# Kernel optimization log

Measured on AMD Instinct MI355X. Metric: run time of the kernel, lower is better.

The kernel has to match this reference:

```python
import jax, jax.numpy as jnp
import numpy as np

C = 128; D_INNER = 256; D_STATE = 16; D_CONV = 4; DT_RANK = 8; SCALE_MLP = 2


def layernorm(x, g, b, eps=1e-5):
    m = x.mean(-1, keepdims=True)
    v = ((x - m) ** 2).mean(-1, keepdims=True)
    return (x - m) * jax.lax.rsqrt(v + eps) * g + b


def causal_conv(x, w, b):
    # x: (B, L, D); w: (D, K) depthwise causal conv; b: (D,)
    K = w.shape[1]
    xt = x.transpose(0, 2, 1)  # (B, D, L)
    out = jax.lax.conv_general_dilated(
        xt, w[:, None, :], (1,), [(K - 1, 0)],
        dimension_numbers=("NCH", "OIH", "NCH"), feature_group_count=w.shape[0])
    return (out + b[None, :, None]).transpose(0, 2, 1)


def selective_scan(u, delta, A, Bm, Cm, Dv):
    # u, delta: (B, L, D); A: (D, N); Bm, Cm: (B, L, N); Dv: (D,)
    def step(h, inp):
        u_t, d_t, B_t, C_t = inp  # (B,D),(B,D),(B,N),(B,N)
        dA = jnp.exp(d_t[..., None] * A)                      # (B, D, N)
        h = dA * h + (d_t * u_t)[..., None] * B_t[:, None, :]  # (B, D, N)
        y = jnp.einsum("bdn,bn->bd", h, C_t)
        return h, y
    Bsz, L, Din = u.shape
    h0 = jnp.zeros((Bsz, Din, A.shape[1]), u.dtype)
    inputs = (u.transpose(1, 0, 2), delta.transpose(1, 0, 2),
              Bm.transpose(1, 0, 2), Cm.transpose(1, 0, 2))
    _, ys = jax.lax.scan(step, h0, inputs)
    return ys.transpose(1, 0, 2) + u * Dv


def mamba_branch(xc, z, cw, cb, Wx_, Wdt_, bdt_, Al, Dv):
    u = jax.nn.silu(causal_conv(xc, cw, cb))
    xdbl = u @ Wx_.T  # (B, L, dt_rank + 2*d_state)
    dr = Wdt_.shape[1]; ds = Al.shape[1]
    dt = jax.nn.softplus(xdbl[..., :dr] @ Wdt_.T + bdt_)
    Bm = xdbl[..., dr:dr + ds]
    Cm = xdbl[..., dr + ds:]
    y = selective_scan(u, dt, -jnp.exp(Al), Bm, Cm, Dv)
    return y * jax.nn.silu(z)


def setup_inputs():
    key = jax.random.key(0)
    ks = jax.random.split(key, 20)
    w = lambda k, shape, s=0.02: jax.random.normal(k, shape, jnp.float32) * s
    A_log = jnp.log(jnp.tile(jnp.arange(1, D_STATE + 1, dtype=jnp.float32), (D_INNER, 1)))
    dt_bias = jnp.full((D_INNER,), jnp.log(jnp.expm1(0.01)), jnp.float32)
    return dict(
        x=jax.random.normal(ks[0], (4, 256, 64, C), jnp.float32),
        g1=jnp.ones((C,), jnp.float32), b1=jnp.zeros((C,), jnp.float32),
        W_in=w(ks[1], (2 * D_INNER, C)),
        conv_w=w(ks[2], (D_INNER, D_CONV), 0.2), conv_b=jnp.zeros((D_INNER,), jnp.float32),
        Wx=w(ks[3], (DT_RANK + 2 * D_STATE, D_INNER)),
        Wdt=w(ks[4], (D_INNER, DT_RANK), 0.1), bdt=dt_bias,
        A_log=A_log, D=jnp.ones((D_INNER,), jnp.float32),
        conv_wb=w(ks[5], (D_INNER, D_CONV), 0.2), conv_bb=jnp.zeros((D_INNER,), jnp.float32),
        Wxb=w(ks[6], (DT_RANK + 2 * D_STATE, D_INNER)),
        Wdtb=w(ks[7], (D_INNER, DT_RANK), 0.1), bdtb=dt_bias,
        A_b_log=A_log, D_b=jnp.ones((D_INNER,), jnp.float32),
        W_out=w(ks[8], (C, D_INNER)),
        g2=jnp.ones((C,), jnp.float32), b2=jnp.zeros((C,), jnp.float32),
        g3=jnp.ones((C,), jnp.float32), b3=jnp.zeros((C,), jnp.float32),
        W1m=w(ks[9], (C, SCALE_MLP * C)), b1m=jnp.zeros((SCALE_MLP * C,), jnp.float32),
        W2m=w(ks[10], (SCALE_MLP * C, C)), b2m=jnp.zeros((C,), jnp.float32),
    )


def reference(x, g1, b1, W_in, conv_w, conv_b, Wx, Wdt, bdt, A_log, D,
              conv_wb, conv_bb, Wxb, Wdtb, bdtb, A_b_log, D_b, W_out,
              g2, b2, g3, b3, W1m, b1m, W2m, b2m):
    B, T, N, Cc = x.shape
    xs = x.transpose(0, 2, 1, 3).reshape(B * N, T, Cc)
    # --- CustomBiMamba: LN -> (Dropout eval=identity) -> BiMamba v2 -> LN, residual ---
    h = layernorm(xs, g1, b1)
    xz = h @ W_in.T  # (B*N, T, 2*d_inner)
    xc, z = jnp.split(xz, 2, axis=-1)
    y_f = mamba_branch(xc, z, conv_w, conv_b, Wx, Wdt, bdt, A_log, D)
    y_b = mamba_branch(xc[:, ::-1], z[:, ::-1], conv_wb, conv_bb, Wxb, Wdtb, bdtb,
                       A_b_log, D_b)[:, ::-1]
    y = (y_f + y_b) @ W_out.T
    y = layernorm(y, g2, b2)
    xs = y + xs
    xo = xs.reshape(B, N, T, Cc).transpose(0, 2, 1, 3)
    # --- MLP residual ---
    h2 = layernorm(xo, g3, b3)
    mlp = jax.nn.gelu(h2 @ W1m + b1m, approximate=False) @ W2m + b2m
    return xo + mlp
```

## Files before the change

kernel.cpp:

```cpp
#include <hip/hip_runtime.h>
#include <hip/hip_bf16.h>
#include <math.h>

#define CC 128
#define DI 256
#define SSEQ 256
#define ROWS 65536

typedef __hip_bfloat16 bf16;
typedef __attribute__((ext_vector_type(8))) short short8;
typedef __attribute__((ext_vector_type(4))) float float4v;
typedef __attribute__((ext_vector_type(2))) float f32x2;

__device__ __forceinline__ float to_f(float v) { return v; }
__device__ __forceinline__ float to_f(bf16 v)  { return __bfloat162float(v); }
__device__ __forceinline__ bf16  f2b(float v)  { return __float2bfloat16(v); }
__device__ __forceinline__ float bf2f_bits(short v) {
    union { unsigned u; float f; } c; c.u = ((unsigned)(unsigned short)v) << 16; return c.f;
}
__device__ __forceinline__ f32x2 mk2(float a, float b) { f32x2 r; r.x = a; r.y = b; return r; }
__device__ __forceinline__ f32x2 fma2(f32x2 a, f32x2 b, f32x2 c) { return a * b + c; }

__device__ __forceinline__ float wave_sum(float v) {
    #pragma unroll
    for (int o = 1; o < 64; o <<= 1) v += __shfl_xor(v, o, 64);
    return v;
}
__device__ __forceinline__ float silu_f(float x) {
    return x * __builtin_amdgcn_rcpf(1.f + __expf(-x));
}
__device__ __forceinline__ float gelu_f(float x) { return 0.5f * x * (1.f + erff(x * 0.70710678118654752f)); }
__device__ __forceinline__ float softplus_f(float x) {
    return (x > 20.f) ? x : __logf(1.f + __expf(x));
}

__global__ __launch_bounds__(256) void ln1_kernel(const float* __restrict__ x,
                                                  const float* __restrict__ g,
                                                  const float* __restrict__ b,
                                                  bf16* __restrict__ out) {
    int wave = threadIdx.x >> 6, lane = threadIdx.x & 63;
    int r = blockIdx.x * 4 + wave;
    int s = r >> 8, t = r & 255;
    int bb = s >> 6, n = s & 63;
    size_t xbase = (((size_t)(bb * 256 + t)) * 64 + n) * CC;
    float v0 = x[xbase + lane], v1 = x[xbase + lane + 64];
    float s1 = wave_sum(v0 + v1);
    float s2 = wave_sum(v0 * v0 + v1 * v1);
    float m = s1 * (1.f / 128.f);
    float var = s2 * (1.f / 128.f) - m * m;
    float rstd = rsqrtf(var + 1e-5f);
    size_t ob = (size_t)r * CC;
    out[ob + lane]      = f2b((v0 - m) * rstd * g[lane]      + b[lane]);
    out[ob + lane + 64] = f2b((v1 - m) * rstd * g[lane + 64] + b[lane + 64]);
// ... 210 lines not shown
        {
            int n = tid >> 2, part = tid & 3;
            if (n < 48) {
                bf16 tmp[8];
                #pragma unroll
                for (int j = 0; j < 8; j++)
                    tmp[j] = (n < 40) ? f2b(Wx[(size_t)n * 256 + k0 + part * 8 + j]) : f2b(0.f);
                *(uint4*)&Bs[n][part * 8] = *(uint4*)tmp;
            }
        }
        __syncthreads();
        short8 a = *(const short8*)&As[wv * 16 + lrow][lk];
        #pragma unroll
        for (int jt = 0; jt < 3; jt++) {
            short8 bfr = *(const short8*)&Bs[jt * 16 + lrow][lk];
            acc[jt] = __builtin_amdgcn_mfma_f32_16x16x32_bf16(a, bfr, acc[jt], 0, 0, 0);
        }
        __syncthreads();
    }
    #pragma unroll
    for (int jt = 0; jt < 3; jt++) {
        int col = jt * 16 + lrow;
        if (col < 40) {
            #pragma unroll
            for (int r = 0; r < 4; r++) {
                int row = t0 + wv * 16 + quad * 4 + r;
                C[(size_t)(s * 256 + row) * 40 + col] = f2b(acc[jt][r]);
            }
        }
    }
}


#define LOADROW(R, T) do {                                                  \
    const float4* rp_ = (const float4*)(rows + (T) * 40);                   \
    R##0 = rp_[0]; R##1 = rp_[1]; R##2 = rp_[2]; R##3 = rp_[3];             \
    R##4 = rp_[4]; R##5 = rp_[5]; R##6 = rp_[6]; R##7 = rp_[7];             \
    R##8 = rp_[8]; R##9 = rp_[9];                                           \
} while (0)

#define SCAN_STEP(T, R) do {                                                \
    float u_ = uc0; uc0 = uc1;                                              \
    if ((T) + 2 < 256) { uc1 = to_f(*unext); unext += ystep; }              \
    f32x2 acc2 = mk2((R##0).x, (R##0).y) * wdt01;                           \
    acc2 = fma2(mk2((R##0).z, (R##0).w), wdt23, acc2);                      \
    acc2 = fma2(mk2((R##1).x, (R##1).y), wdt45, acc2);                      \
    acc2 = fma2(mk2((R##1).z, (R##1).w), wdt67, acc2);                      \
    float dtr_ = bd + acc2.x + acc2.y;                                      \
    float dt_ = softplus_f(dtr_);                                           \
    float du_ = dt_ * u_;                                                   \
    float d1 = __expf(dt_ * A0);                                            \
    float d2v = d1 * d1;                                                    \
    f32x2 pw0 = mk2(d1, d2v);                                               \
    f32x2 dd2 = mk2(d2v, d2v);                                              \
    f32x2 pw1 = pw0 * dd2, pw2 = pw1 * dd2, pw3 = pw2 * dd2;                \
    f32x2 dd8 = mk2(pw3.y, pw3.y);                                          \
    f32x2 pw4 = pw0 * dd8, pw5 = pw1 * dd8, pw6 = pw2 * dd8, pw7 = pw3 * dd8; \
    f32x2 du2 = mk2(du_, du_);                                              \
    hp0 = fma2(pw0, hp0, du2 * mk2((R##2).x, (R##2).y));                    \
    hp1 = fma2(pw1, hp1, du2 * mk2((R##2).z, (R##2).w));                    \
    hp2 = fma2(pw2, hp2, du2 * mk2((R##3).x, (R##3).y));                    \
    hp3 = fma2(pw3, hp3, du2 * mk2((R##3).z, (R##3).w));                    \
    hp4 = fma2(pw4, hp4, du2 * mk2((R##4).x, (R##4).y));                    \
    hp5 = fma2(pw5, hp5, du2 * mk2((R##4).z, (R##4).w));                    \
    hp6 = fma2(pw6, hp6, du2 * mk2((R##5).x, (R##5).y));                    \
    hp7 = fma2(pw7, hp7, du2 * mk2((R##5).z, (R##5).w));                    \
    f32x2 ya = hp0 * mk2((R##6).x, (R##6).y);                               \
    f32x2 yb = hp1 * mk2((R##6).z, (R##6).w);                               \
    ya = fma2(hp2, mk2((R##7).x, (R##7).y), ya);                            \
    yb = fma2(hp3, mk2((R##7).z, (R##7).w), yb);                            \
    ya = fma2(hp4, mk2((R##8).x, (R##8).y), ya);                            \
    yb = fma2(hp5, mk2((R##8).z, (R##8).w), yb);                            \
    ya = fma2(hp6, mk2((R##9).x, (R##9).y), ya);                            \
    yb = fma2(hp7, mk2((R##9).z, (R##9).w), yb);                            \
    f32x2 ys = ya + yb;                                                     \
    float yv_ = ys.x + ys.y + u_ * Dd;                                      \
    *yp = f2b(yv_); yp += ystep;                                            \
} while (0)

__global__ __launch_bounds__(256) void scan_kernel(
        const bf16* __restrict__ xdbl_f, const bf16* __restrict__ xdbl_b,
        const float* __restrict__ Wdt_f, const float* __restrict__ bdt_f,
        const float* __restrict__ Alog_f, const float* __restrict__ D_f,
        const float* __restrict__ Wdt_b, const float* __restrict__ bdt_b,
        const float* __restrict__ Alog_b, const float* __restrict__ D_b,
        bf16* __restrict__ YF, bf16* __restrict__ YB) {
    __shared__ float rows[256 * 40];
    int tid = threadIdx.x;
    int dir = blockIdx.x >> 8;
    int s = blockIdx.x & 255;
    int d = tid;

    const bf16* xd = (dir ? xdbl_b : xdbl_f) + (size_t)s * 10240;
    #pragma unroll
    for (int i = 0; i < 5; i++) {
        int idx = i * 256 + tid;
        uint4 v = ((const uint4*)xd)[idx];
        short8 sv = *(short8*)&v;
        float f[8];
        #pragma unroll
        for (int j = 0; j < 8; j++) f[j] = bf2f_bits(sv[j]);
        *(float4*)&rows[idx * 8]     = *(float4*)&f[0];
        *(float4*)&rows[idx * 8 + 4] = *(float4*)&f[4];
    }

    const float* Alog = dir ? Alog_b : Alog_f;
    const float* Wdtp = dir ? Wdt_b  : Wdt_f;
    float Aarr[16];
    #pragma unroll
    for (int n = 0; n < 16; n++) Aarr[n] = -__expf(Alog[d * 16 + n]);
    f32x2 wdt01 = mk2(Wdtp[d * 8 + 0], Wdtp[d * 8 + 1]);
    f32x2 wdt23 = mk2(Wdtp[d * 8 + 2], Wdtp[d * 8 + 3]);
    f32x2 wdt45 = mk2(Wdtp[d * 8 + 4], Wdtp[d * 8 + 5]);
    f32x2 wdt67 = mk2(Wdtp[d * 8 + 6], Wdtp[d * 8 + 7]);
    float bd = dir ? bdt_b[d] : bdt_f[d];
    float Dd = dir ? D_b[d]   : D_f[d];
    bf16* Y = dir ? YB : YF;

    float A0 = Aarr[0];
    int pw = 1;
    #pragma unroll
    for (int n = 1; n < 16; n++)
        pw &= (fabsf(Aarr[n] - (float)(n + 1) * A0) <= 1e-4f * fabsf(Aarr[n]) + 1e-6f) ? 1 : 0;
    pw = __all(pw);
    __syncthreads();

    bf16* yp = Y + ((size_t)(s * 256 + (dir ? 255 : 0))) * 256 + d;
    ptrdiff_t ystep = dir ? -256 : 256;
    float uc0 = to_f(*yp);
    float uc1 = to_f(*(yp + ystep));
    const bf16* unext = yp + 2 * ystep;

    if (pw) {
        f32x2 hp0 = {}, hp1 = {}, hp2 = {}, hp3 = {},
              hp4 = {}, hp5 = {}, hp6 = {}, hp7 = {};
        float4 ra0, ra1, ra2, ra3, ra4, ra5, ra6, ra7, ra8, ra9;
        float4 rb0, rb1, rb2, rb3, rb4, rb5, rb6, rb7, rb8, rb9;
        LOADROW(ra, 0);
        #pragma unroll 1
        for (int t = 0; t < 256; t += 2) {
            LOADROW(rb, t + 1);
            SCAN_STEP(t, ra);
            if (t + 2 < 256) LOADROW(ra, t + 2);
            SCAN_STEP(t + 1, rb);
        }
    } else {
        float h[16];
        #pragma unroll
        for (int n = 0; n < 16; n++) h[n] = 0.f;
        for (int t = 0; t < 256; t++) {
            float u = uc0; uc0 = uc1;
            if (t + 2 < 256) { uc1 = to_f(*unext); unext += ystep; }
            const float* row = rows + t * 40;
            float4 q0 = *(const float4*)(row);
            float4 q1 = *(const float4*)(row + 4);
            float4 qb0 = *(const float4*)(row + 8);
            float4 qb1 = *(const float4*)(row + 12);
            float4 qb2 = *(const float4*)(row + 16);
            float4 qb3 = *(const float4*)(row + 20);
            float4 qc0 = *(const float4*)(row + 24);
            float4 qc1 = *(const float4*)(row + 28);
            float4 qc2 = *(const float4*)(row + 32);
            float4 qc3 = *(const float4*)(row + 36);
            float dtr = bd;
            dtr += q0.x * wdt01.x + q0.y * wdt01.y + q0.z * wdt23.x + q0.w * wdt23.y;
            dtr += q1.x * wdt45.x + q1.y * wdt45.y + q1.z * wdt67.x + q1.w * wdt67.y;
            float dt = softplus_f(dtr);
            float du = dt * u, y = 0.f;
            float Bm[16] = {qb0.x,qb0.y,qb0.z,qb0.w, qb1.x,qb1.y,qb1.z,qb1.w,
                            qb2.x,qb2.y,qb2.z,qb2.w, qb3.x,qb3.y,qb3.z,qb3.w};
            float Cm[16] = {qc0.x,qc0.y,qc0.z,qc0.w, qc1.x,qc1.y,qc1.z,qc1.w,
                            qc2.x,qc2.y,qc2.z,qc2.w, qc3.x,qc3.y,qc3.z,qc3.w};
            #pragma unroll
            for (int n = 0; n < 16; n++) {
                float dA = __expf(dt * Aarr[n]);
                h[n] = dA * h[n] + du * Bm[n];
                y += h[n] * Cm[n];
            }
            y += u * Dd;
            *yp = f2b(y); yp += ystep;
        }
    }
}

extern "C" void kernel_launch(void* const* d_in, const int* in_sizes, int n_in,
                              void* d_out, int out_size, void* d_ws, size_t ws_size,
                              hipStream_t stream) {
    const float* x      = (const float*)d_in[0];
    const float* g1     = (const float*)d_in[1];
    const float* b1     = (const float*)d_in[2];
    const float* W_in   = (const float*)d_in[3];
    const float* conv_w = (const float*)d_in[4];
    const float* conv_b = (const float*)d_in[5];
    const float* Wx     = (const float*)d_in[6];
    const float* Wdt    = (const float*)d_in[7];
    const float* bdt    = (const float*)d_in[8];
    const float* A_log  = (const float*)d_in[9];
    const float* Dvec   = (const float*)d_in[10];
    const float* conv_wb= (const float*)d_in[11];
    const float* conv_bb= (const float*)d_in[12];
    const float* Wxb    = (const float*)d_in[13];
    const float* Wdtb   = (const float*)d_in[14];
    const float* bdtb   = (const float*)d_in[15];
    const float* A_b_log= (const float*)d_in[16];
    const float* D_b    = (const float*)d_in[17];
    const float* W_out  = (const float*)d_in[18];
    const float* g2     = (const float*)d_in[19];
    const float* b2     = (const float*)d_in[20];
    const float* g3     = (const float*)d_in[21];
    const float* b3     = (const float*)d_in[22];
    const float* W1m    = (const float*)d_in[23];
    const float* b1m    = (const float*)d_in[24];
    const float* W2m    = (const float*)d_in[25];
    const float* b2m    = (const float*)d_in[26];

    bf16* ws  = (bf16*)d_ws;
    bf16* XZ  = ws;
    bf16* YF  = ws + 33554432UL;
    bf16* YB  = ws + 50331648UL;
    bf16* H2  = ws;
    bf16* HID = ws + 8388608UL;
    float* out = (float*)d_out;
    bf16* LN1OUT = (bf16*)d_out;
    bf16* XDBL_F = (bf16*)d_out;
    bf16* XDBL_B = (bf16*)d_out + 2621440UL;

    ln1_kernel<<<ROWS / 4, 256, 0, stream>>>(x, g1, b1, LN1OUT);
    mfma_gemm_kernel<true, 0, 4><<<dim3(ROWS / 64, 8), 256, 0, stream>>>(
        LN1OUT, CC, W_in, nullptr, XZ, 512, 512, CC);
    mfma_conv_kernel<0><<<SSEQ * 4, 256, 0, stream>>>(XZ, conv_w, conv_b, Wx, XDBL_F, YF);
    mfma_conv_kernel<1><<<SSEQ * 4, 256, 0, stream>>>(XZ, conv_wb, conv_bb, Wxb, XDBL_B, YB);
    scan_kernel<<<512, 256, 0, stream>>>(XDBL_F, XDBL_B,
        Wdt, bdt, A_log, Dvec, Wdtb, bdtb, A_b_log, D_b, YF, YB);
    mfma_ln2res_kernel<<<ROWS / 64, 256, 0, stream>>>(YF, YB, XZ, W_out, g2, b2, x, out);
    ln3_kernel<<<ROWS / 4, 256, 0, stream>>>(out, g3, b3, H2);
    mfma_gemm_kernel<false, 1, 4><<<dim3(ROWS / 64, 4), 256, 0, stream>>>(
        H2, CC, W1m, b1m, HID, 2 * CC, 2 * CC, CC);
    mfma_gemm_kernel<false, 2, 8><<<dim3(ROWS / 64, 2), 256, 0, stream>>>(
        HID, 2 * CC, W2m, b2m, out, CC, CC, 2 * CC);
}
```

Measured before the change: 522.7 us.

## Split selective scan into two sequence chunks with a carry-correction pass

The selective scan is split into two 128-step halves per sequence and direction, doubling the block count. The second half starts from a zero state and stores a running prefix sum of dt into a reused scratch region of XZ. The first half stores its final hidden state. A new correction kernel then adds C·exp(A·S)·h_end to the second-half outputs. This trades an extra launch, extra global traffic and a bf16 prefix sum for twice the parallelism on the serial scan, which may cost some accuracy.

```diff
diff --git a/kernel.cpp b/kernel.cpp
--- a/kernel.cpp
+++ b/kernel.cpp
@@ -295,22 +295,23 @@
 }
 
 
-#define LOADROW(R, T) do {                                                  \
-    const float4* rp_ = (const float4*)(rows + (T) * 40);                   \
+#define LOADROW(R, J) do {                                                  \
+    const float4* rp_ = (const float4*)(rows + (J) * 40);                   \
     R##0 = rp_[0]; R##1 = rp_[1]; R##2 = rp_[2]; R##3 = rp_[3];             \
     R##4 = rp_[4]; R##5 = rp_[5]; R##6 = rp_[6]; R##7 = rp_[7];             \
     R##8 = rp_[8]; R##9 = rp_[9];                                           \
 } while (0)
 
-#define SCAN_STEP(T, R) do {                                                \
+#define SCAN_STEP(J, R) do {                                                \
     float u_ = uc0; uc0 = uc1;                                              \
-    if ((T) + 2 < 256) { uc1 = to_f(*unext); unext += ystep; }              \
+    if ((J) + 2 < 128) { uc1 = to_f(*unext); unext += ystep; }              \
     f32x2 acc2 = mk2((R##0).x, (R##0).y) * wdt01;                           \
     acc2 = fma2(mk2((R##0).z, (R##0).w), wdt23, acc2);                      \
     acc2 = fma2(mk2((R##1).x, (R##1).y), wdt45, acc2);                      \
     acc2 = fma2(mk2((R##1).z, (R##1).w), wdt67, acc2);                      \
     float dtr_ = bd + acc2.x + acc2.y;                                      \
     float dt_ = softplus_f(dtr_);                                           \
+    if (kk) { Ssum += dt_; *sp = f2b(Ssum); sp += 512; }                    \
     float du_ = dt_ * u_;                                                   \
     float d1 = __expf(dt_ * A0);                                            \
     float d2v = d1 * d1;                                                    \
@@ -341,30 +342,34 @@
     *yp = f2b(yv_); yp += ystep;                                            \
 } while (0)
 
-__global__ __launch_bounds__(256) void scan_kernel(
+__global__ __launch_bounds__(256, 4) void scan1_kernel(
         const bf16* __restrict__ xdbl_f, const bf16* __restrict__ xdbl_b,
         const float* __restrict__ Wdt_f, const float* __restrict__ bdt_f,
         const float* __restrict__ Alog_f, const float* __restrict__ D_f,
         const float* __restrict__ Wdt_b, const float* __restrict__ bdt_b,
         const float* __restrict__ Alog_b, const float* __restrict__ D_b,
-        bf16* __restrict__ YF, bf16* __restrict__ YB) {
-    __shared__ float rows[256 * 40];
+        bf16* __restrict__ YF, bf16* __restrict__ YB,
+        float* __restrict__ Hend, bf16* __restrict__ Sbuf) {
+    __shared__ float rows[128 * 40];
     int tid = threadIdx.x;
-    int dir = blockIdx.x >> 8;
-    int s = blockIdx.x & 255;
+    int s   = blockIdx.x >> 2;
+    int dir = (blockIdx.x >> 1) & 1;
+    int kk  = blockIdx.x & 1;
     int d = tid;
 
-    const bf16* xd = (dir ? xdbl_b : xdbl_f) + (size_t)s * 10240;
-    #pragma unroll
-    for (int i = 0; i < 5; i++) {
+    const bf16* xd = (dir ? xdbl_b : xdbl_f) + ((size_t)(s * 256 + kk * 128)) * 40;
+    #pragma unroll
+    for (int i = 0; i < 3; i++) {
         int idx = i * 256 + tid;
-        uint4 v = ((const uint4*)xd)[idx];
-        short8 sv = *(short8*)&v;
-        float f[8];
-        #pragma unroll
-        for (int j = 0; j < 8; j++) f[j] = bf2f_bits(sv[j]);
-        *(float4*)&rows[idx * 8]     = *(float4*)&f[0];
-        *(float4*)&rows[idx * 8 + 4] = *(float4*)&f[4];
+        if (idx < 640) {
+            uint4 v = ((const uint4*)xd)[idx];
+            short8 sv = *(short8*)&v;
+            float f[8];
+            #pragma unroll
+            for (int j = 0; j < 8; j++) f[j] = bf2f_bits(sv[j]);
+            *(float4*)&rows[idx * 8]     = *(float4*)&f[0];
+            *(float4*)&rows[idx * 8 + 4] = *(float4*)&f[4];
+        }
     }
 
     const float* Alog = dir ? Alog_b : Alog_f;
@@ -388,11 +393,15 @@
     pw = __all(pw);
     __syncthreads();
 
-    bf16* yp = Y + ((size_t)(s * 256 + (dir ? 255 : 0))) * 256 + d;
+    int row0 = dir ? (255 - kk * 128) : (kk * 128);
+    bf16* yp = Y + ((size_t)(s * 256 + row0)) * 256 + d;
     ptrdiff_t ystep = dir ? -256 : 256;
     float uc0 = to_f(*yp);
     float uc1 = to_f(*(yp + ystep));
     const bf16* unext = yp + 2 * ystep;
+
+    float Ssum = 0.f;
+    bf16* sp = Sbuf + ((size_t)(s * 256 + (dir ? 0 : 128))) * 512 + d;
 
     if (pw) {
         f32x2 hp0 = {}, hp1 = {}, hp2 = {}, hp3 = {},
@@ -401,19 +410,30 @@
         float4 rb0, rb1, rb2, rb3, rb4, rb5, rb6, rb7, rb8, rb9;
         LOADROW(ra, 0);
         #pragma unroll 1
-        for (int t = 0; t < 256; t += 2) {
+        for (int t = 0; t < 128; t += 2) {
             LOADROW(rb, t + 1);
             SCAN_STEP(t, ra);
-            if (t + 2 < 256) LOADROW(ra, t + 2);
+            if (t + 2 < 128) LOADROW(ra, t + 2);
             SCAN_STEP(t + 1, rb);
+        }
+        if (kk == 0) {
+            float* hb = Hend + ((size_t)((dir * 256 + s) * 16)) * 256 + d;
+            hb[0 * 256] = hp0.x; hb[1 * 256] = hp0.y;
+            hb[2 * 256] = hp1.x; hb[3 * 256] = hp1.y;
+            hb[4 * 256] = hp2.x; hb[5 * 256] = hp2.y;
+            hb[6 * 256] = hp3.x; hb[7 * 256] = hp3.y;
+            hb[8 * 256] = hp4.x; hb[9 * 256] = hp4.y;
+            hb[10 * 256] = hp5.x; hb[11 * 256] = hp5.y;
+            hb[12 * 256] = hp6.x; hb[13 * 256] = hp6.y;
+            hb[14 * 256] = hp7.x; hb[15 * 256] = hp7.y;
         }
     } else {
         float h[16];
         #pragma unroll
         for (int n = 0; n < 16; n++) h[n] = 0.f;
-        for (int t = 0; t < 256; t++) {
+        for (int t = 0; t < 128; t++) {
             float u = uc0; uc0 = uc1;
-            if (t + 2 < 256) { uc1 = to_f(*unext); unext += ystep; }
+            if (t + 2 < 128) { uc1 = to_f(*unext); unext += ystep; }
             const float* row = rows + t * 40;
             float4 q0 = *(const float4*)(row);
             float4 q1 = *(const float4*)(row + 4);
@@ -429,6 +449,7 @@
             dtr += q0.x * wdt01.x + q0.y * wdt01.y + q0.z * wdt23.x + q0.w * wdt23.y;
             dtr += q1.x * wdt45.x + q1.y * wdt45.y + q1.z * wdt67.x + q1.w * wdt67.y;
             float dt = softplus_f(dtr);
+            if (kk) { Ssum += dt; *sp = f2b(Ssum); sp += 512; }
             float du = dt * u, y = 0.f;
             float Bm[16] = {qb0.x,qb0.y,qb0.z,qb0.w, qb1.x,qb1.y,qb1.z,qb1.w,
                             qb2.x,qb2.y,qb2.z,qb2.w, qb3.x,qb3.y,qb3.z,qb3.w};
@@ -442,6 +463,100 @@
             }
             y += u * Dd;
             *yp = f2b(y); yp += ystep;
+        }
+        if (kk == 0) {
+            float* hb = Hend + ((size_t)((dir * 256 + s) * 16)) * 256 + d;
+            #pragma unroll
+            for (int n = 0; n < 16; n++) hb[n * 256] = h[n];
+        }
+    }
+}
+
+__global__ __launch_bounds__(256, 4) void scan2_kernel(
+        const bf16* __restrict__ xdbl_f, const bf16* __restrict__ xdbl_b,
+        const float* __restrict__ Alog_f, const float* __restrict__ Alog_b,
+        const float* __restrict__ Hend, const bf16* __restrict__ Sbuf,
+        bf16* __restrict__ YF, bf16* __restrict__ YB) {
+    __shared__ float cms[64 * 16];
+    int tid = threadIdx.x;
+    int s   = blockIdx.x >> 2;
+    int dir = (blockIdx.x >> 1) & 1;
+    int jh  = blockIdx.x & 1;
+    int d = tid;
+
+    const bf16* xd = dir ? xdbl_b : xdbl_f;
+    #pragma unroll
+    for (int i = 0; i < 4; i++) {
+        int e = i * 256 + tid;
+        int j = e >> 4, n = e & 15;
+        cms[j * 16 + n] = to_f(xd[((size_t)(s * 256 + 128 + jh * 64 + j)) * 40 + 24 + n]);
+    }
+
+    const float* Alog = dir ? Alog_b : Alog_f;
+    float Aarr[16];
+    #pragma unroll
+    for (int n = 0; n < 16; n++) Aarr[n] = -__expf(Alog[d * 16 + n]);
+    float A0 = Aarr[0];
+    int pw = 1;
+    #pragma unroll
+    for (int n = 1; n < 16; n++)
+        pw &= (fabsf(Aarr[n] - (float)(n + 1) * A0) <= 1e-4f * fabsf(Aarr[n]) + 1e-6f) ? 1 : 0;
+    pw = __all(pw);
+
+    const float* hb = Hend + ((size_t)((dir * 256 + s) * 16)) * 256 + d;
+    f32x2 H0 = mk2(hb[0 * 256], hb[1 * 256]);
+    f32x2 H1 = mk2(hb[2 * 256], hb[3 * 256]);
+    f32x2 H2 = mk2(hb[4 * 256], hb[5 * 256]);
+    f32x2 H3 = mk2(hb[6 * 256], hb[7 * 256]);
+    f32x2 H4 = mk2(hb[8 * 256], hb[9 * 256]);
+    f32x2 H5 = mk2(hb[10 * 256], hb[11 * 256]);
+    f32x2 H6 = mk2(hb[12 * 256], hb[13 * 256]);
+    f32x2 H7 = mk2(hb[14 * 256], hb[15 * 256]);
+    __syncthreads();
+
+    const bf16* sp = Sbuf + ((size_t)(s * 256 + (dir ? 0 : 128) + jh * 64)) * 512 + d;
+    bf16* Y = dir ? YB : YF;
+    bf16* yp = Y + ((size_t)(s * 256 + (dir ? (127 - jh * 64) : (128 + jh * 64)))) * 256 + d;
+    ptrdiff_t ystep = dir ? -256 : 256;
+
+    if (pw) {
+        #pragma unroll 2
+        for (int j = 0; j < 64; j++) {
+            float S = to_f(sp[(size_t)j * 512]);
+            float e1 = __expf(A0 * S);
+            float e2 = e1 * e1;
+            f32x2 pw0 = mk2(e1, e2);
+            f32x2 dd2 = mk2(e2, e2);
+            f32x2 pw1 = pw0 * dd2, pw2 = pw1 * dd2, pw3 = pw2 * dd2;
+            f32x2 dd8 = mk2(pw3.y, pw3.y);
+            f32x2 pw4 = pw0 * dd8, pw5 = pw1 * dd8, pw6 = pw2 * dd8, pw7 = pw3 * dd8;
+            const float4* cmr = (const float4*)(cms + j * 16);
+            float4 c0 = cmr[0], c1 = cmr[1], c2 = cmr[2], c3 = cmr[3];
+            f32x2 acc = (pw0 * H0) * mk2(c0.x, c0.y);
+            acc = fma2(pw1 * H1, mk2(c0.z, c0.w), acc);
+            acc = fma2(pw2 * H2, mk2(c1.x, c1.y), acc);
+            acc = fma2(pw3 * H3, mk2(c1.z, c1.w), acc);
+            acc = fma2(pw4 * H4, mk2(c2.x, c2.y), acc);
+            acc = fma2(pw5 * H5, mk2(c2.z, c2.w), acc);
+            acc = fma2(pw6 * H6, mk2(c3.x, c3.y), acc);
+            acc = fma2(pw7 * H7, mk2(c3.z, c3.w), acc);
+            float corr = acc.x + acc.y;
+            bf16* ya = yp + (ptrdiff_t)j * ystep;
+            *ya = f2b(to_f(*ya) + corr);
+        }
+    } else {
+        float h0v[16];
+        #pragma unroll
+        for (int n = 0; n < 16; n++) h0v[n] = hb[n * 256];
+        #pragma unroll 2
+        for (int j = 0; j < 64; j++) {
+            float S = to_f(sp[(size_t)j * 512]);
+            float corr = 0.f;
+            #pragma unroll
+            for (int n = 0; n < 16; n++)
+                corr += cms[j * 16 + n] * __expf(Aarr[n] * S) * h0v[n];
+            bf16* ya = yp + (ptrdiff_t)j * ystep;
+            *ya = f2b(to_f(*ya) + corr);
         }
     }
 }
@@ -487,14 +602,17 @@
     bf16* LN1OUT = (bf16*)d_out;
     bf16* XDBL_F = (bf16*)d_out;
     bf16* XDBL_B = (bf16*)d_out + 2621440UL;
+    float* HEND  = (float*)((char*)d_out + (16UL << 20));
 
     ln1_kernel<<<ROWS / 4, 256, 0, stream>>>(x, g1, b1, LN1OUT);
     mfma_gemm_kernel<true, 0, 4><<<dim3(ROWS / 64, 8), 256, 0, stream>>>(
         LN1OUT, CC, W_in, nullptr, XZ, 512, 512, CC);
     mfma_conv_kernel<0><<<SSEQ * 4, 256, 0, stream>>>(XZ, conv_w, conv_b, Wx, XDBL_F, YF);
     mfma_conv_kernel<1><<<SSEQ * 4, 256, 0, stream>>>(XZ, conv_wb, conv_bb, Wxb, XDBL_B, YB);
-    scan_kernel<<<512, 256, 0, stream>>>(XDBL_F, XDBL_B,
-        Wdt, bdt, A_log, Dvec, Wdtb, bdtb, A_b_log, D_b, YF, YB);
+    scan1_kernel<<<1024, 256, 0, stream>>>(XDBL_F, XDBL_B,
+        Wdt, bdt, A_log, Dvec, Wdtb, bdtb, A_b_log, D_b, YF, YB, HEND, XZ);
+    scan2_kernel<<<1024, 256, 0, stream>>>(XDBL_F, XDBL_B, A_log, A_b_log,
+        HEND, XZ, YF, YB);
     mfma_ln2res_kernel<<<ROWS / 64, 256, 0, stream>>>(YF, YB, XZ, W_out, g2, b2, x, out);
     ln3_kernel<<<ROWS / 4, 256, 0, stream>>>(out, g3, b3, H2);
     mfma_gemm_kernel<false, 1, 4><<<dim3(ROWS / 64, 4), 256, 0, stream>>>(
```

After: 698.5 us. 33.6% more time.

## Split selective scan over two sequence halves with carry-state correction pass

Applied to the files above, without the earlier changes.

The scan kernel now uses 512 threads per block, with each half of the threads scanning 128 timesteps of the sequence from a zero state. The first half writes its final hidden state to shared memory. The second half then runs a correction pass that decays this carried state through its own steps and adds the C-weighted contribution to its outputs. The aim is to double the parallelism of the sequential scan on a launch that has only 512 blocks. The cost is recomputing dt and the decays and rereading and rewriting the second-half outputs, and the correction pass runs serially after the barrier.

```diff
diff --git a/kernel.cpp b/kernel.cpp
--- a/kernel.cpp
+++ b/kernel.cpp
@@ -302,9 +302,9 @@
     R##8 = rp_[8]; R##9 = rp_[9];                                           \
 } while (0)
 
-#define SCAN_STEP(T, R) do {                                                \
+#define SCAN_STEP(J, R) do {                                                \
     float u_ = uc0; uc0 = uc1;                                              \
-    if ((T) + 2 < 256) { uc1 = to_f(*unext); unext += ystep; }              \
+    if ((J) + 2 < 128) { uc1 = to_f(*unext); unext += ystep; }              \
     f32x2 acc2 = mk2((R##0).x, (R##0).y) * wdt01;                           \
     acc2 = fma2(mk2((R##0).z, (R##0).w), wdt23, acc2);                      \
     acc2 = fma2(mk2((R##1).x, (R##1).y), wdt45, acc2);                      \
@@ -329,19 +329,19 @@
     hp6 = fma2(pw6, hp6, du2 * mk2((R##5).x, (R##5).y));                    \
     hp7 = fma2(pw7, hp7, du2 * mk2((R##5).z, (R##5).w));                    \
     f32x2 ya = hp0 * mk2((R##6).x, (R##6).y);                               \
-    f32x2 yb = hp1 * mk2((R##6).z, (R##6).w);                               \
+    f32x2 yb2 = hp1 * mk2((R##6).z, (R##6).w);                              \
     ya = fma2(hp2, mk2((R##7).x, (R##7).y), ya);                            \
-    yb = fma2(hp3, mk2((R##7).z, (R##7).w), yb);                            \
+    yb2 = fma2(hp3, mk2((R##7).z, (R##7).w), yb2);                          \
     ya = fma2(hp4, mk2((R##8).x, (R##8).y), ya);                            \
-    yb = fma2(hp5, mk2((R##8).z, (R##8).w), yb);                            \
+    yb2 = fma2(hp5, mk2((R##8).z, (R##8).w), yb2);                          \
     ya = fma2(hp6, mk2((R##9).x, (R##9).y), ya);                            \
-    yb = fma2(hp7, mk2((R##9).z, (R##9).w), yb);                            \
-    f32x2 ys = ya + yb;                                                     \
+    yb2 = fma2(hp7, mk2((R##9).z, (R##9).w), yb2);                          \
+    f32x2 ys = ya + yb2;                                                    \
     float yv_ = ys.x + ys.y + u_ * Dd;                                      \
     *yp = f2b(yv_); yp += ystep;                                            \
 } while (0)
 
-__global__ __launch_bounds__(256) void scan_kernel(
+__global__ __launch_bounds__(512, 4) void scan_kernel(
         const bf16* __restrict__ xdbl_f, const bf16* __restrict__ xdbl_b,
         const float* __restrict__ Wdt_f, const float* __restrict__ bdt_f,
         const float* __restrict__ Alog_f, const float* __restrict__ D_f,
@@ -349,22 +349,26 @@
         const float* __restrict__ Alog_b, const float* __restrict__ D_b,
         bf16* __restrict__ YF, bf16* __restrict__ YB) {
     __shared__ float rows[256 * 40];
+    __shared__ float hbuf[16 * 256];
     int tid = threadIdx.x;
     int dir = blockIdx.x >> 8;
     int s = blockIdx.x & 255;
-    int d = tid;
+    int half = tid >> 8;
+    int d = tid & 255;
 
     const bf16* xd = (dir ? xdbl_b : xdbl_f) + (size_t)s * 10240;
     #pragma unroll
-    for (int i = 0; i < 5; i++) {
-        int idx = i * 256 + tid;
-        uint4 v = ((const uint4*)xd)[idx];
-        short8 sv = *(short8*)&v;
-        float f[8];
-        #pragma unroll
-        for (int j = 0; j < 8; j++) f[j] = bf2f_bits(sv[j]);
-        *(float4*)&rows[idx * 8]     = *(float4*)&f[0];
-        *(float4*)&rows[idx * 8 + 4] = *(float4*)&f[4];
+    for (int i = 0; i < 3; i++) {
+        int idx = i * 512 + tid;
+        if (idx < 1280) {
+            uint4 v = ((const uint4*)xd)[idx];
+            short8 sv = *(short8*)&v;
+            float f[8];
+            #pragma unroll
+            for (int j = 0; j < 8; j++) f[j] = bf2f_bits(sv[j]);
+            *(float4*)&rows[idx * 8]     = *(float4*)&f[0];
+            *(float4*)&rows[idx * 8 + 4] = *(float4*)&f[4];
+        }
     }
 
     const float* Alog = dir ? Alog_b : Alog_f;
@@ -388,7 +392,9 @@
     pw = __all(pw);
     __syncthreads();
 
-    bf16* yp = Y + ((size_t)(s * 256 + (dir ? 255 : 0))) * 256 + d;
+    int t0 = half * 128;
+    int row0 = dir ? (255 - t0) : t0;
+    bf16* yp = Y + ((size_t)(s * 256 + row0)) * 256 + d;
     ptrdiff_t ystep = dir ? -256 : 256;
     float uc0 = to_f(*yp);
     float uc1 = to_f(*(yp + ystep));
@@ -399,49 +405,125 @@
               hp4 = {}, hp5 = {}, hp6 = {}, hp7 = {};
         float4 ra0, ra1, ra2, ra3, ra4, ra5, ra6, ra7, ra8, ra9;
         float4 rb0, rb1, rb2, rb3, rb4, rb5, rb6, rb7, rb8, rb9;
-        LOADROW(ra, 0);
+        LOADROW(ra, t0);
         #pragma unroll 1
-        for (int t = 0; t < 256; t += 2) {
-            LOADROW(rb, t + 1);
-            SCAN_STEP(t, ra);
-            if (t + 2 < 256) LOADROW(ra, t + 2);
-            SCAN_STEP(t + 1, rb);
+        for (int j = 0; j < 128; j += 2) {
+            LOADROW(rb, t0 + j + 1);
+            SCAN_STEP(j, ra);
+            if (j + 2 < 128) LOADROW(ra, t0 + j + 2);
+            SCAN_STEP(j + 1, rb);
+        }
+        if (half == 0) {
+            hbuf[0 * 256 + d]  = hp0.x; hbuf[1 * 256 + d]  = hp0.y;
+            hbuf[2 * 256 + d]  = hp1.x; hbuf[3 * 256 + d]  = hp1.y;
+            hbuf[4 * 256 + d]  = hp2.x; hbuf[5 * 256 + d]  = hp2.y;
+            hbuf[6 * 256 + d]  = hp3.x; hbuf[7 * 256 + d]  = hp3.y;
+            hbuf[8 * 256 + d]  = hp4.x; hbuf[9 * 256 + d]  = hp4.y;
+            hbuf[10 * 256 + d] = hp5.x; hbuf[11 * 256 + d] = hp5.y;
+            hbuf[12 * 256 + d] = hp6.x; hbuf[13 * 256 + d] = hp6.y;
+            hbuf[14 * 256 + d] = hp7.x; hbuf[15 * 256 + d] = hp7.y;
+        }
+        __syncthreads();
+        if (half == 1) {
+            f32x2 g0 = mk2(hbuf[0 * 256 + d],  hbuf[1 * 256 + d]);
+            f32x2 g1 = mk2(hbuf[2 * 256 + d],  hbuf[3 * 256 + d]);
+            f32x2 g2 = mk2(hbuf[4 * 256 + d],  hbuf[5 * 256 + d]);
+            f32x2 g3 = mk2(hbuf[6 * 256 + d],  hbuf[7 * 256 + d]);
+            f32x2 g4 = mk2(hbuf[8 * 256 + d],  hbuf[9 * 256 + d]);
+            f32x2 g5 = mk2(hbuf[10 * 256 + d], hbuf[11 * 256 + d]);
+            f32x2 g6 = mk2(hbuf[12 * 256 + d], hbuf[13 * 256 + d]);
+            f32x2 g7 = mk2(hbuf[14 * 256 + d], hbuf[15 * 256 + d]);
+            bf16* yb = Y + ((size_t)(s * 256 + (dir ? 127 : 128))) * 256 + d;
+            float yc0 = to_f(*yb);
+            float yc1 = to_f(*(yb + ystep));
+            const bf16* ynext = yb + 2 * ystep;
+            #pragma unroll 1
+            for (int j = 0; j < 128; j++) {
+                const float* row = rows + (128 + j) * 40;
+                float4 q0 = *(const float4*)(row);
+                float4 q1 = *(const float4*)(row + 4);
+                f32x2 acc2 = mk2(q0.x, q0.y) * wdt01;
+                acc2 = fma2(mk2(q0.z, q0.w), wdt23, acc2);
+                acc2 = fma2(mk2(q1.x, q1.y), wdt45, acc2);
+                acc2 = fma2(mk2(q1.z, q1.w), wdt67, acc2);
+                float dt = softplus_f(bd + acc2.x + acc2.y);
+                float e1 = __expf(dt * A0);
+                float e2 = e1 * e1;
+                f32x2 pp0 = mk2(e1, e2);
+                f32x2 dd2 = mk2(e2, e2);
+                f32x2 pp1 = pp0 * dd2, pp2 = pp1 * dd2, pp3 = pp2 * dd2;
+                f32x2 dd8 = mk2(pp3.y, pp3.y);
+                f32x2 pp4 = pp0 * dd8, pp5 = pp1 * dd8, pp6 = pp2 * dd8, pp7 = pp3 * dd8;
+                g0 = pp0 * g0; g1 = pp1 * g1; g2 = pp2 * g2; g3 = pp3 * g3;
+                g4 = pp4 * g4; g5 = pp5 * g5; g6 = pp6 * g6; g7 = pp7 * g7;
+                const float4* cmr = (const float4*)(row + 24);
+                float4 c0 = cmr[0], c1 = cmr[1], c2 = cmr[2], c3 = cmr[3];
+                f32x2 acc = g0 * mk2(c0.x, c0.y);
+                acc = fma2(g1, mk2(c0.z, c0.w), acc);
+                acc = fma2(g2, mk2(c1.x, c1.y), acc);
+                acc = fma2(g3, mk2(c1.z, c1.w), acc);
+                acc = fma2(g4, mk2(c2.x, c2.y), acc);
+                acc = fma2(g5, mk2(c2.z, c2.w), acc);
+                acc = fma2(g6, mk2(c3.x, c3.y), acc);
+                acc = fma2(g7, mk2(c3.z, c3.w), acc);
+                float ynew = yc0 + acc.x + acc.y;
+                yc0 = yc1;
+                if (j + 2 < 128) { yc1 = to_f(*ynext); ynext += ystep; }
+                *yb = f2b(ynew); yb += ystep;
+            }
         }
     } else {
         float h[16];
         #pragma unroll
         for (int n = 0; n < 16; n++) h[n] = 0.f;
-        for (int t = 0; t < 256; t++) {
+        #pragma unroll 1
+        for (int j = 0; j < 128; j++) {
             float u = uc0; uc0 = uc1;
-            if (t + 2 < 256) { uc1 = to_f(*unext); unext += ystep; }
-            const float* row = rows + t * 40;
+            if (j + 2 < 128) { uc1 = to_f(*unext); unext += ystep; }
+            const float* row = rows + (t0 + j) * 40;
             float4 q0 = *(const float4*)(row);
             float4 q1 = *(const float4*)(row + 4);
-            float4 qb0 = *(const float4*)(row + 8);
-            float4 qb1 = *(const float4*)(row + 12);
-            float4 qb2 = *(const float4*)(row + 16);
-            float4 qb3 = *(const float4*)(row + 20);
-            float4 qc0 = *(const float4*)(row + 24);
-            float4 qc1 = *(const float4*)(row + 28);
-            float4 qc2 = *(const float4*)(row + 32);
-            float4 qc3 = *(const float4*)(row + 36);
             float dtr = bd;
             dtr += q0.x * wdt01.x + q0.y * wdt01.y + q0.z * wdt23.x + q0.w * wdt23.y;
             dtr += q1.x * wdt45.x + q1.y * wdt45.y + q1.z * wdt67.x + q1.w * wdt67.y;
             float dt = softplus_f(dtr);
             float du = dt * u, y = 0.f;
-            float Bm[16] = {qb0.x,qb0.y,qb0.z,qb0.w, qb1.x,qb1.y,qb1.z,qb1.w,
-                            qb2.x,qb2.y,qb2.z,qb2.w, qb3.x,qb3.y,qb3.z,qb3.w};
-            float Cm[16] = {qc0.x,qc0.y,qc0.z,qc0.w, qc1.x,qc1.y,qc1.z,qc1.w,
-                            qc2.x,qc2.y,qc2.z,qc2.w, qc3.x,qc3.y,qc3.z,qc3.w};
             #pragma unroll
             for (int n = 0; n < 16; n++) {
                 float dA = __expf(dt * Aarr[n]);
-                h[n] = dA * h[n] + du * Bm[n];
-                y += h[n] * Cm[n];
+                h[n] = dA * h[n] + du * row[8 + n];
+                y += h[n] * row[24 + n];
             }
             y += u * Dd;
             *yp = f2b(y); yp += ystep;
+        }
+        if (half == 0) {
+            #pragma unroll
+            for (int n = 0; n < 16; n++) hbuf[n * 256 + d] = h[n];
+        }
+        __syncthreads();
+        if (half == 1) {
+            float g[16];
+            #pragma unroll
+            for (int n = 0; n < 16; n++) g[n] = hbuf[n * 256 + d];
+            bf16* yb = Y + ((size_t)(s * 256 + (dir ? 127 : 128))) * 256 + d;
+            #pragma unroll 1
+            for (int j = 0; j < 128; j++) {
+                const float* row = rows + (128 + j) * 40;
+                float4 q0 = *(const float4*)(row);
+                float4 q1 = *(const float4*)(row + 4);
+                float dtr = bd;
+                dtr += q0.x * wdt01.x + q0.y * wdt01.y + q0.z * wdt23.x + q0.w * wdt23.y;
+                dtr += q1.x * wdt45.x + q1.y * wdt45.y + q1.z * wdt67.x + q1.w * wdt67.y;
+                float dt = softplus_f(dtr);
+                float corr = 0.f;
+                #pragma unroll
+                for (int n = 0; n < 16; n++) {
+                    g[n] *= __expf(dt * Aarr[n]);
+                    corr += g[n] * row[24 + n];
+                }
+                *yb = f2b(to_f(*yb) + corr); yb += ystep;
+            }
         }
     }
 }
@@ -493,7 +575,7 @@
         LN1OUT, CC, W_in, nullptr, XZ, 512, 512, CC);
     mfma_conv_kernel<0><<<SSEQ * 4, 256, 0, stream>>>(XZ, conv_w, conv_b, Wx, XDBL_F, YF);
     mfma_conv_kernel<1><<<SSEQ * 4, 256, 0, stream>>>(XZ, conv_wb, conv_bb, Wxb, XDBL_B, YB);
-    scan_kernel<<<512, 256, 0, stream>>>(XDBL_F, XDBL_B,
+    scan_kernel<<<512, 512, 0, stream>>>(XDBL_F, XDBL_B,
         Wdt, bdt, A_log, Dvec, Wdtb, bdtb, A_b_log, D_b, YF, YB);
     mfma_ln2res_kernel<<<ROWS / 64, 256, 0, stream>>>(YF, YB, XZ, W_out, g2, b2, x, out);
     ln3_kernel<<<ROWS / 4, 256, 0, stream>>>(out, g3, b3, H2);
```

Measured after the change: 556.1 us. 1.06x slower.

## Split selective scan into four time chunks with carry propagation pass

Applied to the files above, without the earlier changes.

The scan kernel now runs 1024 threads per block, splitting the 256-step sequence into four 64-step chunks processed in parallel. Each chunk first scans from zero state; final states are then propagated serially through shared memory using the cumulative decay exp(A*sum(dt)), and chunks 1-3 rerun a correction pass that adds the decayed carried-in state's contribution to their outputs. The xdbl rows are also kept as bf16 in shared memory and converted on use instead of being expanded to fp32 up front. This raises parallelism in the latency-bound serial scan, in exchange for roughly doubling the arithmetic for later chunks, extra global read-modify-write of Y, and block-wide synchronisation.

```diff
diff --git a/kernel.cpp b/kernel.cpp
--- a/kernel.cpp
+++ b/kernel.cpp
@@ -18,7 +18,14 @@
 __device__ __forceinline__ float bf2f_bits(short v) {
     union { unsigned u; float f; } c; c.u = ((unsigned)(unsigned short)v) << 16; return c.f;
 }
+__device__ __forceinline__ float blo(unsigned w) {
+    union { unsigned u; float f; } c; c.u = w << 16; return c.f;
+}
+__device__ __forceinline__ float bhi(unsigned w) {
+    union { unsigned u; float f; } c; c.u = w & 0xffff0000u; return c.f;
+}
 __device__ __forceinline__ f32x2 mk2(float a, float b) { f32x2 r; r.x = a; r.y = b; return r; }
+__device__ __forceinline__ f32x2 bp2(unsigned w) { return mk2(blo(w), bhi(w)); }
 __device__ __forceinline__ f32x2 fma2(f32x2 a, f32x2 b, f32x2 c) { return a * b + c; }
 
 __device__ __forceinline__ float wave_sum(float v) {
@@ -295,76 +302,26 @@
 }
 
 
-#define LOADROW(R, T) do {                                                  \
-    const float4* rp_ = (const float4*)(rows + (T) * 40);                   \
-    R##0 = rp_[0]; R##1 = rp_[1]; R##2 = rp_[2]; R##3 = rp_[3];             \
-    R##4 = rp_[4]; R##5 = rp_[5]; R##6 = rp_[6]; R##7 = rp_[7];             \
-    R##8 = rp_[8]; R##9 = rp_[9];                                           \
-} while (0)
-
-#define SCAN_STEP(T, R) do {                                                \
-    float u_ = uc0; uc0 = uc1;                                              \
-    if ((T) + 2 < 256) { uc1 = to_f(*unext); unext += ystep; }              \
-    f32x2 acc2 = mk2((R##0).x, (R##0).y) * wdt01;                           \
-    acc2 = fma2(mk2((R##0).z, (R##0).w), wdt23, acc2);                      \
-    acc2 = fma2(mk2((R##1).x, (R##1).y), wdt45, acc2);                      \
-    acc2 = fma2(mk2((R##1).z, (R##1).w), wdt67, acc2);                      \
-    float dtr_ = bd + acc2.x + acc2.y;                                      \
-    float dt_ = softplus_f(dtr_);                                           \
-    float du_ = dt_ * u_;                                                   \
-    float d1 = __expf(dt_ * A0);                                            \
-    float d2v = d1 * d1;                                                    \
-    f32x2 pw0 = mk2(d1, d2v);                                               \
-    f32x2 dd2 = mk2(d2v, d2v);                                              \
-    f32x2 pw1 = pw0 * dd2, pw2 = pw1 * dd2, pw3 = pw2 * dd2;                \
-    f32x2 dd8 = mk2(pw3.y, pw3.y);                                          \
-    f32x2 pw4 = pw0 * dd8, pw5 = pw1 * dd8, pw6 = pw2 * dd8, pw7 = pw3 * dd8; \
-    f32x2 du2 = mk2(du_, du_);                                              \
-    hp0 = fma2(pw0, hp0, du2 * mk2((R##2).x, (R##2).y));                    \
-    hp1 = fma2(pw1, hp1, du2 * mk2((R##2).z, (R##2).w));                    \
-    hp2 = fma2(pw2, hp2, du2 * mk2((R##3).x, (R##3).y));                    \
-    hp3 = fma2(pw3, hp3, du2 * mk2((R##3).z, (R##3).w));                    \
-    hp4 = fma2(pw4, hp4, du2 * mk2((R##4).x, (R##4).y));                    \
-    hp5 = fma2(pw5, hp5, du2 * mk2((R##4).z, (R##4).w));                    \
-    hp6 = fma2(pw6, hp6, du2 * mk2((R##5).x, (R##5).y));                    \
-    hp7 = fma2(pw7, hp7, du2 * mk2((R##5).z, (R##5).w));                    \
-    f32x2 ya = hp0 * mk2((R##6).x, (R##6).y);                               \
-    f32x2 yb = hp1 * mk2((R##6).z, (R##6).w);                               \
-    ya = fma2(hp2, mk2((R##7).x, (R##7).y), ya);                            \
-    yb = fma2(hp3, mk2((R##7).z, (R##7).w), yb);                            \
-    ya = fma2(hp4, mk2((R##8).x, (R##8).y), ya);                            \
-    yb = fma2(hp5, mk2((R##8).z, (R##8).w), yb);                            \
-    ya = fma2(hp6, mk2((R##9).x, (R##9).y), ya);                            \
-    yb = fma2(hp7, mk2((R##9).z, (R##9).w), yb);                            \
-    f32x2 ys = ya + yb;                                                     \
-    float yv_ = ys.x + ys.y + u_ * Dd;                                      \
-    *yp = f2b(yv_); yp += ystep;                                            \
-} while (0)
-
-__global__ __launch_bounds__(256) void scan_kernel(
+__global__ __launch_bounds__(1024, 8) void scan_kernel(
         const bf16* __restrict__ xdbl_f, const bf16* __restrict__ xdbl_b,
         const float* __restrict__ Wdt_f, const float* __restrict__ bdt_f,
         const float* __restrict__ Alog_f, const float* __restrict__ D_f,
         const float* __restrict__ Wdt_b, const float* __restrict__ bdt_b,
         const float* __restrict__ Alog_b, const float* __restrict__ D_b,
         bf16* __restrict__ YF, bf16* __restrict__ YB) {
-    __shared__ float rows[256 * 40];
+    __shared__ unsigned rowsw[256 * 20];
+    __shared__ float hbuf[16 * 256];
     int tid = threadIdx.x;
     int dir = blockIdx.x >> 8;
     int s = blockIdx.x & 255;
-    int d = tid;
+    int ck = tid >> 8;
+    int d = tid & 255;
 
     const bf16* xd = (dir ? xdbl_b : xdbl_f) + (size_t)s * 10240;
     #pragma unroll
-    for (int i = 0; i < 5; i++) {
-        int idx = i * 256 + tid;
-        uint4 v = ((const uint4*)xd)[idx];
-        short8 sv = *(short8*)&v;
-        float f[8];
-        #pragma unroll
-        for (int j = 0; j < 8; j++) f[j] = bf2f_bits(sv[j]);
-        *(float4*)&rows[idx * 8]     = *(float4*)&f[0];
-        *(float4*)&rows[idx * 8 + 4] = *(float4*)&f[4];
+    for (int i = 0; i < 2; i++) {
+        int idx = i * 1024 + tid;
+        if (idx < 1280) ((uint4*)rowsw)[idx] = ((const uint4*)xd)[idx];
     }
 
     const float* Alog = dir ? Alog_b : Alog_f;
@@ -388,60 +345,196 @@
     pw = __all(pw);
     __syncthreads();
 
-    bf16* yp = Y + ((size_t)(s * 256 + (dir ? 255 : 0))) * 256 + d;
+    int t0 = ck * 64;
+    int row0 = dir ? (255 - t0) : t0;
+    bf16* yp = Y + ((size_t)(s * 256 + row0)) * 256 + d;
     ptrdiff_t ystep = dir ? -256 : 256;
     float uc0 = to_f(*yp);
     float uc1 = to_f(*(yp + ystep));
     const bf16* unext = yp + 2 * ystep;
+    float Ssum = 0.f;
+    float he[16];
 
     if (pw) {
         f32x2 hp0 = {}, hp1 = {}, hp2 = {}, hp3 = {},
               hp4 = {}, hp5 = {}, hp6 = {}, hp7 = {};
-        float4 ra0, ra1, ra2, ra3, ra4, ra5, ra6, ra7, ra8, ra9;
-        float4 rb0, rb1, rb2, rb3, rb4, rb5, rb6, rb7, rb8, rb9;
-        LOADROW(ra, 0);
-        #pragma unroll 1
-        for (int t = 0; t < 256; t += 2) {
-            LOADROW(rb, t + 1);
-            SCAN_STEP(t, ra);
-            if (t + 2 < 256) LOADROW(ra, t + 2);
-            SCAN_STEP(t + 1, rb);
-        }
+        #pragma unroll 2
+        for (int j = 0; j < 64; j++) {
+            float u_ = uc0; uc0 = uc1;
+            if (j + 2 < 64) { uc1 = to_f(*unext); unext += ystep; }
+            const uint4* rp = (const uint4*)rowsw + (size_t)(t0 + j) * 5;
+            uint4 qw = rp[0], bw0 = rp[1], bw1 = rp[2], cw0 = rp[3], cw1 = rp[4];
+            f32x2 a2 = bp2(qw.x) * wdt01;
+            a2 = fma2(bp2(qw.y), wdt23, a2);
+            a2 = fma2(bp2(qw.z), wdt45, a2);
+            a2 = fma2(bp2(qw.w), wdt67, a2);
+            float dt_ = softplus_f(bd + a2.x + a2.y);
+            Ssum += dt_;
+            float du_ = dt_ * u_;
+            float d1 = __expf(dt_ * A0);
+            float d2v = d1 * d1;
+            f32x2 pw0 = mk2(d1, d2v);
+            f32x2 dd2 = mk2(d2v, d2v);
+            f32x2 pw1 = pw0 * dd2, pw2 = pw1 * dd2, pw3 = pw2 * dd2;
+            f32x2 dd8 = mk2(pw3.y, pw3.y);
+            f32x2 pw4 = pw0 * dd8, pw5 = pw1 * dd8, pw6 = pw2 * dd8, pw7 = pw3 * dd8;
+            f32x2 du2 = mk2(du_, du_);
+            hp0 = fma2(pw0, hp0, du2 * bp2(bw0.x));
+            hp1 = fma2(pw1, hp1, du2 * bp2(bw0.y));
+            hp2 = fma2(pw2, hp2, du2 * bp2(bw0.z));
+            hp3 = fma2(pw3, hp3, du2 * bp2(bw0.w));
+            hp4 = fma2(pw4, hp4, du2 * bp2(bw1.x));
+            hp5 = fma2(pw5, hp5, du2 * bp2(bw1.y));
+            hp6 = fma2(pw6, hp6, du2 * bp2(bw1.z));
+            hp7 = fma2(pw7, hp7, du2 * bp2(bw1.w));
+            f32x2 ya = hp0 * bp2(cw0.x);
+            f32x2 yb2 = hp1 * bp2(cw0.y);
+            ya = fma2(hp2, bp2(cw0.z), ya);
+            yb2 = fma2(hp3, bp2(cw0.w), yb2);
+            ya = fma2(hp4, bp2(cw1.x), ya);
+            yb2 = fma2(hp5, bp2(cw1.y), yb2);
+            ya = fma2(hp6, bp2(cw1.z), ya);
+            yb2 = fma2(hp7, bp2(cw1.w), yb2);
+            f32x2 ys = ya + yb2;
+            *yp = f2b(ys.x + ys.y + u_ * Dd);
+            yp += ystep;
+        }
+        he[0] = hp0.x;  he[1] = hp0.y;  he[2] = hp1.x;  he[3] = hp1.y;
+        he[4] = hp2.x;  he[5] = hp2.y;  he[6] = hp3.x;  he[7] = hp3.y;
+        he[8] = hp4.x;  he[9] = hp4.y;  he[10] = hp5.x; he[11] = hp5.y;
+        he[12] = hp6.x; he[13] = hp6.y; he[14] = hp7.x; he[15] = hp7.y;
     } else {
         float h[16];
         #pragma unroll
         for (int n = 0; n < 16; n++) h[n] = 0.f;
-        for (int t = 0; t < 256; t++) {
+        #pragma unroll 1
+        for (int j = 0; j < 64; j++) {
             float u = uc0; uc0 = uc1;
-            if (t + 2 < 256) { uc1 = to_f(*unext); unext += ystep; }
-            const float* row = rows + t * 40;
-            float4 q0 = *(const float4*)(row);
-            float4 q1 = *(const float4*)(row + 4);
-            float4 qb0 = *(const float4*)(row + 8);
-            float4 qb1 = *(const float4*)(row + 12);
-            float4 qb2 = *(const float4*)(row + 16);
-            float4 qb3 = *(const float4*)(row + 20);
-            float4 qc0 = *(const float4*)(row + 24);
-            float4 qc1 = *(const float4*)(row + 28);
-            float4 qc2 = *(const float4*)(row + 32);
-            float4 qc3 = *(const float4*)(row + 36);
+            if (j + 2 < 64) { uc1 = to_f(*unext); unext += ystep; }
+            const unsigned short* rw = (const unsigned short*)rowsw + (size_t)(t0 + j) * 40;
             float dtr = bd;
-            dtr += q0.x * wdt01.x + q0.y * wdt01.y + q0.z * wdt23.x + q0.w * wdt23.y;
-            dtr += q1.x * wdt45.x + q1.y * wdt45.y + q1.z * wdt67.x + q1.w * wdt67.y;
+            #pragma unroll
+            for (int i = 0; i < 4; i++) {
+                f32x2 w2 = (i == 0) ? wdt01 : (i == 1) ? wdt23 : (i == 2) ? wdt45 : wdt67;
+                dtr += bf2f_bits(rw[2 * i]) * w2.x + bf2f_bits(rw[2 * i + 1]) * w2.y;
+            }
             float dt = softplus_f(dtr);
+            Ssum += dt;
             float du = dt * u, y = 0.f;
-            float Bm[16] = {qb0.x,qb0.y,qb0.z,qb0.w, qb1.x,qb1.y,qb1.z,qb1.w,
-                            qb2.x,qb2.y,qb2.z,qb2.w, qb3.x,qb3.y,qb3.z,qb3.w};
-            float Cm[16] = {qc0.x,qc0.y,qc0.z,qc0.w, qc1.x,qc1.y,qc1.z,qc1.w,
-                            qc2.x,qc2.y,qc2.z,qc2.w, qc3.x,qc3.y,qc3.z,qc3.w};
             #pragma unroll
             for (int n = 0; n < 16; n++) {
                 float dA = __expf(dt * Aarr[n]);
-                h[n] = dA * h[n] + du * Bm[n];
-                y += h[n] * Cm[n];
+                h[n] = dA * h[n] + du * bf2f_bits(rw[8 + n]);
+                y += h[n] * bf2f_bits(rw[24 + n]);
             }
             y += u * Dd;
             *yp = f2b(y); yp += ystep;
+        }
+        #pragma unroll
+        for (int n = 0; n < 16; n++) he[n] = h[n];
+    }
+
+    float gg[16];
+    float pf[16];
+    if (ck == 1 || ck == 2) {
+        if (pw) {
+            float p1 = __expf(A0 * Ssum);
+            pf[0] = p1;
+            #pragma unroll
+            for (int n = 1; n < 16; n++) pf[n] = pf[n - 1] * p1;
+        } else {
+            #pragma unroll
+            for (int n = 0; n < 16; n++) pf[n] = __expf(Aarr[n] * Ssum);
+        }
+    }
+    __syncthreads();
+    if (ck == 0) {
+        #pragma unroll
+        for (int n = 0; n < 16; n++) hbuf[n * 256 + d] = he[n];
+    }
+    __syncthreads();
+    if (ck == 1) {
+        #pragma unroll
+        for (int n = 0; n < 16; n++) gg[n] = hbuf[n * 256 + d];
+        #pragma unroll
+        for (int n = 0; n < 16; n++) hbuf[n * 256 + d] = he[n] + pf[n] * gg[n];
+    }
+    __syncthreads();
+    if (ck == 2) {
+        #pragma unroll
+        for (int n = 0; n < 16; n++) gg[n] = hbuf[n * 256 + d];
+        #pragma unroll
+        for (int n = 0; n < 16; n++) hbuf[n * 256 + d] = he[n] + pf[n] * gg[n];
+    }
+    __syncthreads();
+    if (ck == 3) {
+        #pragma unroll
+        for (int n = 0; n < 16; n++) gg[n] = hbuf[n * 256 + d];
+    }
+
+    if (ck >= 1) {
+        bf16* yb = Y + ((size_t)(s * 256 + row0)) * 256 + d;
+        float yc0 = to_f(*yb);
+        float yc1 = to_f(*(yb + ystep));
+        const bf16* ynext = yb + 2 * ystep;
+        if (pw) {
+            f32x2 g0 = mk2(gg[0], gg[1]),   g1 = mk2(gg[2], gg[3]);
+            f32x2 g2 = mk2(gg[4], gg[5]),   g3 = mk2(gg[6], gg[7]);
+            f32x2 g4 = mk2(gg[8], gg[9]),   g5 = mk2(gg[10], gg[11]);
+            f32x2 g6 = mk2(gg[12], gg[13]), g7 = mk2(gg[14], gg[15]);
+            #pragma unroll 2
+            for (int j = 0; j < 64; j++) {
+                const uint4* rp = (const uint4*)rowsw + (size_t)(t0 + j) * 5;
+                uint4 qw = rp[0], cw0 = rp[3], cw1 = rp[4];
+                f32x2 a2 = bp2(qw.x) * wdt01;
+                a2 = fma2(bp2(qw.y), wdt23, a2);
+                a2 = fma2(bp2(qw.z), wdt45, a2);
+                a2 = fma2(bp2(qw.w), wdt67, a2);
+                float dt = softplus_f(bd + a2.x + a2.y);
+                float e1 = __expf(dt * A0);
+                float e2 = e1 * e1;
+                f32x2 pp0 = mk2(e1, e2);
+                f32x2 dd2 = mk2(e2, e2);
+                f32x2 pp1 = pp0 * dd2, pp2 = pp1 * dd2, pp3 = pp2 * dd2;
+                f32x2 dd8 = mk2(pp3.y, pp3.y);
+                f32x2 pp4 = pp0 * dd8, pp5 = pp1 * dd8, pp6 = pp2 * dd8, pp7 = pp3 * dd8;
+                g0 = pp0 * g0; g1 = pp1 * g1; g2 = pp2 * g2; g3 = pp3 * g3;
+                g4 = pp4 * g4; g5 = pp5 * g5; g6 = pp6 * g6; g7 = pp7 * g7;
+                f32x2 acc = g0 * bp2(cw0.x);
+                acc = fma2(g1, bp2(cw0.y), acc);
+                acc = fma2(g2, bp2(cw0.z), acc);
+                acc = fma2(g3, bp2(cw0.w), acc);
+                acc = fma2(g4, bp2(cw1.x), acc);
+                acc = fma2(g5, bp2(cw1.y), acc);
+                acc = fma2(g6, bp2(cw1.z), acc);
+                acc = fma2(g7, bp2(cw1.w), acc);
+                float ynew = yc0 + acc.x + acc.y;
+                yc0 = yc1;
+                if (j + 2 < 64) { yc1 = to_f(*ynext); ynext += ystep; }
+                *yb = f2b(ynew); yb += ystep;
+            }
+        } else {
+            #pragma unroll 1
+            for (int j = 0; j < 64; j++) {
+                const unsigned short* rw = (const unsigned short*)rowsw + (size_t)(t0 + j) * 40;
+                float dtr = bd;
+                #pragma unroll
+                for (int i = 0; i < 4; i++) {
+                    f32x2 w2 = (i == 0) ? wdt01 : (i == 1) ? wdt23 : (i == 2) ? wdt45 : wdt67;
+                    dtr += bf2f_bits(rw[2 * i]) * w2.x + bf2f_bits(rw[2 * i + 1]) * w2.y;
+                }
+                float dt = softplus_f(dtr);
+                float corr = 0.f;
+                #pragma unroll
+                for (int n = 0; n < 16; n++) {
+                    gg[n] *= __expf(dt * Aarr[n]);
+                    corr += gg[n] * bf2f_bits(rw[24 + n]);
+                }
+                float ynew = yc0 + corr;
+                yc0 = yc1;
+                if (j + 2 < 64) { yc1 = to_f(*ynext); ynext += ystep; }
+                *yb = f2b(ynew); yb += ystep;
+            }
         }
     }
 }
@@ -493,7 +586,7 @@
         LN1OUT, CC, W_in, nullptr, XZ, 512, 512, CC);
     mfma_conv_kernel<0><<<SSEQ * 4, 256, 0, stream>>>(XZ, conv_w, conv_b, Wx, XDBL_F, YF);
     mfma_conv_kernel<1><<<SSEQ * 4, 256, 0, stream>>>(XZ, conv_wb, conv_bb, Wxb, XDBL_B, YB);
-    scan_kernel<<<512, 256, 0, stream>>>(XDBL_F, XDBL_B,
+    scan_kernel<<<512, 1024, 0, stream>>>(XDBL_F, XDBL_B,
         Wdt, bdt, A_log, Dvec, Wdtb, bdtb, A_b_log, D_b, YF, YB);
     mfma_ln2res_kernel<<<ROWS / 64, 256, 0, stream>>>(YF, YB, XZ, W_out, g2, b2, x, out);
     ln3_kernel<<<ROWS / 4, 256, 0, stream>>>(out, g3, b3, H2);
```

New measurement: 606.8 us. 16.1% more time.
